# Kernel optimization log

Measured on AMD Instinct MI355X. Metric: run time of the kernel, lower is better.

Reference implementation:

```python
import jax, jax.numpy as jnp
import numpy as np
from jax import lax

B, N, D = 8, 1024, 2
MAX_ITERS = 100
REG = 0.1
INNER = 10  # convergence check cadence (cpt % 10 == 0 in the torch code)
TOL = 1e-3


def setup_inputs() -> dict:
    key = jax.random.key(0)
    k1, k2, k3, k4 = jax.random.split(key, 4)
    return {
        "coord1": jax.random.normal(k1, (B, N, D), jnp.float32),
        "prob1": jax.random.uniform(k2, (B, N), jnp.float32),
        "coord2": jax.random.normal(k3, (B, N, D), jnp.float32),
        "prob2": jax.random.uniform(k4, (B, N), jnp.float32),
    }


def _pairwise_sq(x, y):
    # squared euclidean distance, [B, N, N]; same math as the torch cat/broadcast version
    return jnp.sum((x[:, :, None, :] - y[:, None, :, :]) ** 2, axis=-1)


def _sinkhorn(a, b, M):
    bsz, n = a.shape
    a = a[..., None]                      # [B, n, 1]
    b = b[..., None]                      # [B, n, 1]
    K = jnp.exp(-M / REG)                 # [B, n, n]
    Kt = jnp.swapaxes(K, 1, 2)
    u0 = jnp.full((bsz, n, 1), 1.0 / n, M.dtype)
    v0 = jnp.full((bsz, n, 1), 1.0 / n, M.dtype)
    P0 = u0 * K * jnp.swapaxes(v0, 1, 2)
    done0 = jnp.array(False)

    def inner(c, _):
        u, v, done = c
        KtU = jnp.matmul(Kt, u)           # [B, n, 1]
        v1 = b / KtU
        u1 = a / jnp.matmul(K, v1)
        bad = jnp.any(KtU == 0) | ~(jnp.all(jnp.isfinite(u1)) & jnp.all(jnp.isfinite(v1)))
        ok = ~(done | bad)                # freeze updates after break (numerical error)
        return (jnp.where(ok, u1, u), jnp.where(ok, v1, v), done | bad), None

    def outer(c, _):
        u, v, P, done = c
        (u, v, done2), _ = lax.scan(inner, (u, v, done), None, length=INNER)
        Pn = u * K * jnp.swapaxes(v, 1, 2)
        upd = ~done2                      # skip P update if bad/converged already
        conv = jnp.max(jnp.abs(P - Pn)) < TOL
        P = jnp.where(upd, Pn, P)
        return (u, v, P, done2 | (upd & conv)), None

    (_, _, P, _), _ = lax.scan(outer, (u0, v0, P0, done0), None, length=MAX_ITERS // INNER)
    return P


def reference(coord1, prob1, coord2, prob2):
    M = _pairwise_sq(coord1, coord2)
    M = M / jnp.max(M, axis=(1, 2), keepdims=True)
    a = prob1 + 1e-8
    a = a / jnp.sum(a, axis=1, keepdims=True)
    bb = prob2 + 1e-8
    bb = bb / jnp.sum(bb, axis=1, keepdims=True)
    return _sinkhorn(a, bb, M)
```

## Files before the change

### kernel.cpp

```cpp
#include <hip/hip_runtime.h>
#include <hip/hip_fp16.h>

#define NPTS 1024
#define BATCH 8
#define BPB 32
#define NBLOCKS (BATCH * BPB)
#define NTHREADS 512
#define WPB 8
#define RPW 4
#define KCH 16
#define KP  8

#define SCOPE_AGENT __HIP_MEMORY_SCOPE_AGENT

typedef unsigned long long ull;

constexpr float REG_ = 0.1f;
constexpr float LOG2E = 1.4426950408889634f;
constexpr unsigned POISON = 0xAAAAAAAAu;

__device__ __forceinline__ float wave_sum(float x) {
    #pragma unroll
    for (int off = 32; off; off >>= 1) x += __shfl_xor(x, off);
    return x;
}
__device__ __forceinline__ float wave_max(float x) {
    #pragma unroll
    for (int off = 32; off; off >>= 1) x = fmaxf(x, __shfl_xor(x, off));
    return x;
}

__global__ __launch_bounds__(NTHREADS, 2) void sinkhorn_fused(
    const float2* __restrict__ c1g, const float* __restrict__ p1g,
    const float2* __restrict__ c2g, const float* __restrict__ p2g,
    float* __restrict__ out, unsigned* __restrict__ cnt_all,
    int* __restrict__ mmw_all, ull* __restrict__ upk_all,
    ull* __restrict__ vpk_all)
{
    const int tid  = threadIdx.x;
    const int lane = tid & 63;
    const int w    = tid >> 6;
    const int bid  = blockIdx.x & (BATCH - 1);
    const int sub  = blockIdx.x >> 3;
    const int gb   = bid << 10;
    const int r0   = sub * 32 + w * RPW;

    unsigned* cnt = cnt_all + bid * 32;
    int*      mmw = mmw_all + bid * 32;
    ull* upk = upk_all + (gb >> 1);
    ull* vpk = vpk_all + (gb >> 1);

    __shared__ float xe[NPTS];
    __shared__ float red[WPB];
    __shared__ float smax;

    float s1 = 0.f, s2 = 0.f;
    #pragma unroll
    for (int k = 0; k < KCH; ++k) {
        int t = lane + 64 * k;
        s1 += p1g[gb + t] + 1e-8f;
        s2 += p2g[gb + t] + 1e-8f;
    }
    s1 = wave_sum(s1);
    s2 = wave_sum(s2);

    float rc1x[RPW], rc1y[RPW], rc2x[RPW], rc2y[RPW], pa[RPW], pb[RPW];
    #pragma unroll
    for (int i = 0; i < RPW; ++i) {
        float2 c1 = c1g[gb + r0 + i];
        float2 c2 = c2g[gb + r0 + i];
        rc1x[i] = c1.x; rc1y[i] = c1.y;
        rc2x[i] = c2.x; rc2y[i] = c2.y;
        pa[i] = (p1g[gb + r0 + i] + 1e-8f) / s1;
        pb[i] = (p2g[gb + r0 + i] + 1e-8f) / s2;
    }

    float m = 0.f;
    #pragma unroll
    for (int k = 0; k < KCH; ++k) {
        float2 c = c2g[gb + lane + 64 * k];
        #pragma unroll
        for (int i = 0; i < RPW; ++i) {
            float dx = rc1x[i] - c.x, dy = rc1y[i] - c.y;
            m = fmaxf(m, dx * dx + dy * dy);
        }
    }
    m = wave_max(m);
    if (lane == 0) red[w] = m;
    __syncthreads();

    unsigned tgt = POISON + BPB;
    if (tid == 0) {
        float bm = red[0];
        #pragma unroll
        for (int i = 1; i < WPB; ++i) bm = fmaxf(bm, red[i]);
        __hip_atomic_fetch_max(mmw, (int)__float_as_uint(bm),
                               __ATOMIC_RELAXED, SCOPE_AGENT);
        asm volatile("s_waitcnt vmcnt(0)" ::: "memory");
        __hip_atomic_fetch_add(cnt, 1u, __ATOMIC_RELAXED, SCOPE_AGENT);
        while ((int)(__hip_atomic_load(cnt, __ATOMIC_RELAXED, SCOPE_AGENT) - tgt) < 0) {}
        smax = __uint_as_float((unsigned)
            __hip_atomic_load(mmw, __ATOMIC_RELAXED, SCOPE_AGENT));
    }
    __syncthreads();
    const float mmax = smax;
    const float nIL2 = -LOG2E / (REG_ * mmax);

    __half2 Kupk[RPW][KP], Kvpk[RPW][KP];
    #pragma unroll
    for (int p = 0; p < KP; ++p) {
        float2 cA = c2g[gb + lane + 128 * p];
        float2 cB = c2g[gb + lane + 128 * p + 64];
        #pragma unroll
        for (int i = 0; i < RPW; ++i) {
            float dxa = rc1x[i] - cA.x, dya = rc1y[i] - cA.y;
            float dxb = rc1x[i] - cB.x, dyb = rc1y[i] - cB.y;
            Kupk[i][p] = __floats2half2_rn(exp2f(nIL2 * (dxa * dxa + dya * dya)),
                                           exp2f(nIL2 * (dxb * dxb + dyb * dyb)));
        }
        float2 cC = c1g[gb + lane + 128 * p];
        float2 cD = c1g[gb + lane + 128 * p + 64];
        #pragma unroll
        for (int i = 0; i < RPW; ++i) {
            float dxa = rc2x[i] - cC.x, dya = rc2y[i] - cC.y;
            float dxb = rc2x[i] - cD.x, dyb = rc2y[i] - cD.y;
            Kvpk[i][p] = __floats2half2_rn(exp2f(nIL2 * (dxa * dxa + dya * dya)),
                                           exp2f(nIL2 * (dxb * dxb + dyb * dyb)));
        }
    }

    const int sa = (w << 6) + lane;
    float accu[RPW];
    float vcp[KCH];
    for (int it = 0; it < 10; ++it) {
        float acc[RPW] = {0.f, 0.f, 0.f, 0.f};
        if (it == 0) {
            #pragma unroll
            for (int p = 0; p < KP; ++p)
                #pragma unroll
                for (int i = 0; i < RPW; ++i) {
                    float2 kf = __half22float2(Kvpk[i][p]);
                    acc[i] += kf.x + kf.y;
                }
            #pragma unroll
            for (int i = 0; i < RPW; ++i) acc[i] *= (1.0f / NPTS);
        } else {
            #pragma unroll
            for (int p = 0; p < KP; ++p) {
                float x0 = xe[128 * p + lane];
                float x1 = xe[128 * p + 64 + lane];
                #pragma unroll
                for (int i = 0; i < RPW; ++i) {
                    float2 kf = __half22float2(Kvpk[i][p]);
                    acc[i] = fmaf(kf.x, x0, fmaf(kf.y, x1, acc[i]));
                }
            }
        }
        #pragma unroll
        for (int i = 0; i < RPW; ++i) acc[i] = wave_sum(acc[i]);
        if (lane == 0) {
            float v0 = pb[0] / acc[0], v1 = pb[1] / acc[1];
            float v2 = pb[2] / acc[2], v3 = pb[3] / acc[3];
            __hip_atomic_store(&vpk[r0 >> 1],
                ((ull)__float_as_uint(v1) << 32) | __float_as_uint(v0),
                __ATOMIC_RELAXED, SCOPE_AGENT);
            __hip_atomic_store(&vpk[(r0 >> 1) + 1],
                ((ull)__float_as_uint(v3) << 32) | __float_as_uint(v2),
                __ATOMIC_RELAXED, SCOPE_AGENT);
        }
        __syncthreads();
        tgt += BPB;
        if (tid == 0) {
            __hip_atomic_fetch_add(cnt, 1u, __ATOMIC_RELAXED, SCOPE_AGENT);
            while ((int)(__hip_atomic_load(cnt, __ATOMIC_RELAXED, SCOPE_AGENT) - tgt) < 0) {}
        }
        __syncthreads();
        {
            ull r = __hip_atomic_load(&vpk[sa], __ATOMIC_RELAXED, SCOPE_AGENT);
            ((float2*)xe)[sa] = make_float2(__uint_as_float((unsigned)r),
                                            __uint_as_float((unsigned)(r >> 32)));
        }
        __syncthreads();

        #pragma unroll
        for (int i = 0; i < RPW; ++i) accu[i] = 0.f;
        #pragma unroll
        for (int p = 0; p < KP; ++p) {
            float x0 = xe[128 * p + lane];
            float x1 = xe[128 * p + 64 + lane];
            if (it == 9) { vcp[2 * p] = x0; vcp[2 * p + 1] = x1; }
            #pragma unroll
            for (int i = 0; i < RPW; ++i) {
                float2 kf = __half22float2(Kupk[i][p]);
                accu[i] = fmaf(kf.x, x0, fmaf(kf.y, x1, accu[i]));
            }
        }
        #pragma unroll
        for (int i = 0; i < RPW; ++i) accu[i] = wave_sum(accu[i]);
        if (it < 9) {
            if (lane == 0) {
                float u0 = pa[0] / accu[0], u1 = pa[1] / accu[1];
                float u2 = pa[2] / accu[2], u3 = pa[3] / accu[3];
                __hip_atomic_store(&upk[r0 >> 1],
                    ((ull)__float_as_uint(u1) << 32) | __float_as_uint(u0),
                    __ATOMIC_RELAXED, SCOPE_AGENT);
                __hip_atomic_store(&upk[(r0 >> 1) + 1],
                    ((ull)__float_as_uint(u3) << 32) | __float_as_uint(u2),
                    __ATOMIC_RELAXED, SCOPE_AGENT);
            }
            __syncthreads();
            tgt += BPB;
            if (tid == 0) {
                __hip_atomic_fetch_add(cnt, 1u, __ATOMIC_RELAXED, SCOPE_AGENT);
                while ((int)(__hip_atomic_load(cnt, __ATOMIC_RELAXED, SCOPE_AGENT) - tgt) < 0) {}
            }
            __syncthreads();
            ull r = __hip_atomic_load(&upk[sa], __ATOMIC_RELAXED, SCOPE_AGENT);
            ((float2*)xe)[sa] = make_float2(__uint_as_float((unsigned)r),
                                            __uint_as_float((unsigned)(r >> 32)));
            __syncthreads();
        }
    }

    float rowu[RPW];
    #pragma unroll
    for (int i = 0; i < RPW; ++i) rowu[i] = pa[i] / accu[i];
    const long ob = ((long)bid << 20) + ((long)r0 << 10);
    #pragma unroll
    for (int p = 0; p < KP; ++p) {
        #pragma unroll
        for (int i = 0; i < RPW; ++i) {
            float2 kf = __half22float2(Kupk[i][p]);
            __builtin_nontemporal_store(rowu[i] * kf.x * vcp[2 * p],
                &out[ob + (i << 10) + 128 * p + lane]);
            __builtin_nontemporal_store(rowu[i] * kf.y * vcp[2 * p + 1],
                &out[ob + (i << 10) + 128 * p + 64 + lane]);
        }
    }
}

extern "C" void kernel_launch(void* const* d_in, const int* in_sizes, int n_in,
                              void* d_out, int out_size, void* d_ws, size_t ws_size,
                              hipStream_t stream) {
    const float2* c1 = (const float2*)d_in[0];
    const float*  p1 = (const float*)d_in[1];
    const float2* c2 = (const float2*)d_in[2];
    const float*  p2 = (const float*)d_in[3];
    float* out = (float*)d_out;

    unsigned* cnt = (unsigned*)d_ws;
    int*      mmw = (int*)((char*)d_ws + 1024);
    ull* upk = (ull*)((char*)d_ws + 2048);
    ull* vpk = upk + BATCH * NPTS / 2;

    sinkhorn_fused<<<NBLOCKS, NTHREADS, 0, stream>>>(c1, p1, c2, p2, out,
                                                     cnt, mmw, upk, vpk);
}
```

Before: 120.3 us.

## Replace counter barriers with tagged per-element flags and double-buffered shared vectors

Drops the per-batch atomic counter barrier and its three block syncs per half-iteration. Each u/v value is now published as a 64-bit word that carries an iteration tag, and every thread spins only on the two elements it needs. The shared exchange buffer is double-buffered, so a single __syncthreads is enough per exchange. This takes counter contention and serialized barrier latency off the critical path, at the cost of many more polling loads. It also assumes the workspace contents never accidentally match the tags (it depends on workspace initialisation state across calls).

```diff
diff --git a/kernel.cpp b/kernel.cpp
--- a/kernel.cpp
+++ b/kernel.cpp
@@ -17,7 +17,7 @@
 
 constexpr float REG_ = 0.1f;
 constexpr float LOG2E = 1.4426950408889634f;
-constexpr unsigned POISON = 0xAAAAAAAAu;
+constexpr unsigned MTAG = 0xBEEFu;
 
 __device__ __forceinline__ float wave_sum(float x) {
     #pragma unroll
@@ -28,14 +28,22 @@
     #pragma unroll
     for (int off = 32; off; off >>= 1) x = fmaxf(x, __shfl_xor(x, off));
     return x;
+}
+__device__ __forceinline__ ull pk(float v, unsigned tag) {
+    return ((ull)__float_as_uint(v) << 32) | (ull)tag;
+}
+__device__ __forceinline__ ull aload(const ull* p) {
+    return __hip_atomic_load(p, __ATOMIC_RELAXED, SCOPE_AGENT);
+}
+__device__ __forceinline__ void astore(ull* p, ull v) {
+    __hip_atomic_store(p, v, __ATOMIC_RELAXED, SCOPE_AGENT);
 }
 
 __global__ __launch_bounds__(NTHREADS, 2) void sinkhorn_fused(
     const float2* __restrict__ c1g, const float* __restrict__ p1g,
     const float2* __restrict__ c2g, const float* __restrict__ p2g,
-    float* __restrict__ out, unsigned* __restrict__ cnt_all,
-    int* __restrict__ mmw_all, ull* __restrict__ upk_all,
-    ull* __restrict__ vpk_all)
+    float* __restrict__ out, ull* __restrict__ mx_all,
+    ull* __restrict__ vat_all, ull* __restrict__ uat_all)
 {
     const int tid  = threadIdx.x;
     const int lane = tid & 63;
@@ -45,14 +53,12 @@
     const int gb   = bid << 10;
     const int r0   = sub * 32 + w * RPW;
 
-    unsigned* cnt = cnt_all + bid * 32;
-    int*      mmw = mmw_all + bid * 32;
-    ull* upk = upk_all + (gb >> 1);
-    ull* vpk = vpk_all + (gb >> 1);
-
-    __shared__ float xe[NPTS];
+    ull* mx  = mx_all  + bid * 32;
+    ull* vat = vat_all + gb;
+    ull* uat = uat_all + gb;
+
+    __shared__ float xe[2][NPTS];
     __shared__ float red[WPB];
-    __shared__ float smax;
 
     float s1 = 0.f, s2 = 0.f;
     #pragma unroll
@@ -88,22 +94,19 @@
     m = wave_max(m);
     if (lane == 0) red[w] = m;
     __syncthreads();
-
-    unsigned tgt = POISON + BPB;
     if (tid == 0) {
         float bm = red[0];
         #pragma unroll
         for (int i = 1; i < WPB; ++i) bm = fmaxf(bm, red[i]);
-        __hip_atomic_fetch_max(mmw, (int)__float_as_uint(bm),
-                               __ATOMIC_RELAXED, SCOPE_AGENT);
-        asm volatile("s_waitcnt vmcnt(0)" ::: "memory");
-        __hip_atomic_fetch_add(cnt, 1u, __ATOMIC_RELAXED, SCOPE_AGENT);
-        while ((int)(__hip_atomic_load(cnt, __ATOMIC_RELAXED, SCOPE_AGENT) - tgt) < 0) {}
-        smax = __uint_as_float((unsigned)
-            __hip_atomic_load(mmw, __ATOMIC_RELAXED, SCOPE_AGENT));
-    }
-    __syncthreads();
-    const float mmax = smax;
+        astore(mx + sub, pk(bm, MTAG));
+    }
+    float mmax;
+    {
+        const ull* p = mx + (lane & 31);
+        ull r = aload(p);
+        while ((unsigned)r != MTAG) r = aload(p);
+        mmax = wave_max(__uint_as_float((unsigned)(r >> 32)));
+    }
     const float nIL2 = -LOG2E / (REG_ * mmax);
 
     __half2 Kupk[RPW][KP], Kvpk[RPW][KP];
@@ -129,10 +132,13 @@
         }
     }
 
-    const int sa = (w << 6) + lane;
+    const int j2 = 2 * tid;
+    int cb = 0;
     float accu[RPW];
     float vcp[KCH];
     for (int it = 0; it < 10; ++it) {
+        const unsigned tg = (unsigned)(it + 1);
+
         float acc[RPW] = {0.f, 0.f, 0.f, 0.f};
         if (it == 0) {
             #pragma unroll
@@ -147,8 +153,8 @@
         } else {
             #pragma unroll
             for (int p = 0; p < KP; ++p) {
-                float x0 = xe[128 * p + lane];
-                float x1 = xe[128 * p + 64 + lane];
+                float x0 = xe[cb][128 * p + lane];
+                float x1 = xe[cb][128 * p + 64 + lane];
                 #pragma unroll
                 for (int i = 0; i < RPW; ++i) {
                     float2 kf = __half22float2(Kvpk[i][p]);
@@ -158,36 +164,27 @@
         }
         #pragma unroll
         for (int i = 0; i < RPW; ++i) acc[i] = wave_sum(acc[i]);
-        if (lane == 0) {
-            float v0 = pb[0] / acc[0], v1 = pb[1] / acc[1];
-            float v2 = pb[2] / acc[2], v3 = pb[3] / acc[3];
-            __hip_atomic_store(&vpk[r0 >> 1],
-                ((ull)__float_as_uint(v1) << 32) | __float_as_uint(v0),
-                __ATOMIC_RELAXED, SCOPE_AGENT);
-            __hip_atomic_store(&vpk[(r0 >> 1) + 1],
-                ((ull)__float_as_uint(v3) << 32) | __float_as_uint(v2),
-                __ATOMIC_RELAXED, SCOPE_AGENT);
+        if (lane < RPW) {
+            float num = lane == 0 ? pb[0] : lane == 1 ? pb[1] : lane == 2 ? pb[2] : pb[3];
+            float den = lane == 0 ? acc[0] : lane == 1 ? acc[1] : lane == 2 ? acc[2] : acc[3];
+            astore(vat + r0 + lane, pk(num / den, tg));
+        }
+        {
+            ull a = aload(vat + j2), b = aload(vat + j2 + 1);
+            while ((unsigned)a != tg) a = aload(vat + j2);
+            while ((unsigned)b != tg) b = aload(vat + j2 + 1);
+            xe[cb ^ 1][j2]     = __uint_as_float((unsigned)(a >> 32));
+            xe[cb ^ 1][j2 + 1] = __uint_as_float((unsigned)(b >> 32));
         }
         __syncthreads();
-        tgt += BPB;
-        if (tid == 0) {
-            __hip_atomic_fetch_add(cnt, 1u, __ATOMIC_RELAXED, SCOPE_AGENT);
-            while ((int)(__hip_atomic_load(cnt, __ATOMIC_RELAXED, SCOPE_AGENT) - tgt) < 0) {}
-        }
-        __syncthreads();
-        {
-            ull r = __hip_atomic_load(&vpk[sa], __ATOMIC_RELAXED, SCOPE_AGENT);
-            ((float2*)xe)[sa] = make_float2(__uint_as_float((unsigned)r),
-                                            __uint_as_float((unsigned)(r >> 32)));
-        }
-        __syncthreads();
+        cb ^= 1;
 
         #pragma unroll
         for (int i = 0; i < RPW; ++i) accu[i] = 0.f;
         #pragma unroll
         for (int p = 0; p < KP; ++p) {
-            float x0 = xe[128 * p + lane];
-            float x1 = xe[128 * p + 64 + lane];
+            float x0 = xe[cb][128 * p + lane];
+            float x1 = xe[cb][128 * p + 64 + lane];
             if (it == 9) { vcp[2 * p] = x0; vcp[2 * p + 1] = x1; }
             #pragma unroll
             for (int i = 0; i < RPW; ++i) {
@@ -198,27 +195,18 @@
         #pragma unroll
         for (int i = 0; i < RPW; ++i) accu[i] = wave_sum(accu[i]);
         if (it < 9) {
-            if (lane == 0) {
-                float u0 = pa[0] / accu[0], u1 = pa[1] / accu[1];
-                float u2 = pa[2] / accu[2], u3 = pa[3] / accu[3];
-                __hip_atomic_store(&upk[r0 >> 1],
-                    ((ull)__float_as_uint(u1) << 32) | __float_as_uint(u0),
-                    __ATOMIC_RELAXED, SCOPE_AGENT);
-                __hip_atomic_store(&upk[(r0 >> 1) + 1],
-                    ((ull)__float_as_uint(u3) << 32) | __float_as_uint(u2),
-                    __ATOMIC_RELAXED, SCOPE_AGENT);
+            if (lane < RPW) {
+                float num = lane == 0 ? pa[0] : lane == 1 ? pa[1] : lane == 2 ? pa[2] : pa[3];
+                float den = lane == 0 ? accu[0] : lane == 1 ? accu[1] : lane == 2 ? accu[2] : accu[3];
+                astore(uat + r0 + lane, pk(num / den, tg));
             }
+            ull a = aload(uat + j2), b = aload(uat + j2 + 1);
+            while ((unsigned)a != tg) a = aload(uat + j2);
+            while ((unsigned)b != tg) b = aload(uat + j2 + 1);
+            xe[cb ^ 1][j2]     = __uint_as_float((unsigned)(a >> 32));
+            xe[cb ^ 1][j2 + 1] = __uint_as_float((unsigned)(b >> 32));
             __syncthreads();
-            tgt += BPB;
-            if (tid == 0) {
-                __hip_atomic_fetch_add(cnt, 1u, __ATOMIC_RELAXED, SCOPE_AGENT);
-                while ((int)(__hip_atomic_load(cnt, __ATOMIC_RELAXED, SCOPE_AGENT) - tgt) < 0) {}
-            }
-            __syncthreads();
-            ull r = __hip_atomic_load(&upk[sa], __ATOMIC_RELAXED, SCOPE_AGENT);
-            ((float2*)xe)[sa] = make_float2(__uint_as_float((unsigned)r),
-                                            __uint_as_float((unsigned)(r >> 32)));
-            __syncthreads();
+            cb ^= 1;
         }
     }
 
@@ -248,11 +236,10 @@
     const float*  p2 = (const float*)d_in[3];
     float* out = (float*)d_out;
 
-    unsigned* cnt = (unsigned*)d_ws;
-    int*      mmw = (int*)((char*)d_ws + 1024);
-    ull* upk = (ull*)((char*)d_ws + 2048);
-    ull* vpk = upk + BATCH * NPTS / 2;
+    ull* mx  = (ull*)d_ws;
+    ull* vat = (ull*)((char*)d_ws + 2048);
+    ull* uat = vat + BATCH * NPTS;
 
     sinkhorn_fused<<<NBLOCKS, NTHREADS, 0, stream>>>(c1, p1, c2, p2, out,
-                                                     cnt, mmw, upk, vpk);
-}
+                                                     mx, vat, uat);
+}
```

Result: slower. 157.5 us (+30.9%).

## Split per-batch grid barrier counter into four padded counters polled by one wave

Applied to the files above, without the earlier changes.

Replaces the single per-batch atomic barrier counter with four counters, each on its own 128-byte slot and each shared by eight blocks. Waiting is done by lanes of wave 0 polling all four counters in parallel, so fewer atomic increments land on the same address. The per-row u/v divisions and packed stores are also split across two lanes instead of one. The aim is less atomic serialisation at the barrier, at the cost of more polling traffic and a new workspace layout.

```diff
diff --git a/kernel.cpp b/kernel.cpp
--- a/kernel.cpp
+++ b/kernel.cpp
@@ -10,6 +10,7 @@
 #define RPW 4
 #define KCH 16
 #define KP  8
+#define NCTR 4
 
 #define SCOPE_AGENT __HIP_MEMORY_SCOPE_AGENT
 
@@ -28,14 +29,23 @@
     #pragma unroll
     for (int off = 32; off; off >>= 1) x = fmaxf(x, __shfl_xor(x, off));
     return x;
+}
+__device__ __forceinline__ ull aload(const ull* p) {
+    return __hip_atomic_load(p, __ATOMIC_RELAXED, SCOPE_AGENT);
+}
+__device__ __forceinline__ void astore(ull* p, ull v) {
+    __hip_atomic_store(p, v, __ATOMIC_RELAXED, SCOPE_AGENT);
+}
+__device__ __forceinline__ unsigned aload32(const unsigned* p) {
+    return __hip_atomic_load(p, __ATOMIC_RELAXED, SCOPE_AGENT);
 }
 
 __global__ __launch_bounds__(NTHREADS, 2) void sinkhorn_fused(
     const float2* __restrict__ c1g, const float* __restrict__ p1g,
     const float2* __restrict__ c2g, const float* __restrict__ p2g,
     float* __restrict__ out, unsigned* __restrict__ cnt_all,
-    int* __restrict__ mmw_all, ull* __restrict__ upk_all,
-    ull* __restrict__ vpk_all)
+    int* __restrict__ mmw_all, unsigned* __restrict__ pc_all,
+    ull* __restrict__ upk_all, ull* __restrict__ vpk_all)
 {
     const int tid  = threadIdx.x;
     const int lane = tid & 63;
@@ -47,6 +57,7 @@
 
     unsigned* cnt = cnt_all + bid * 32;
     int*      mmw = mmw_all + bid * 32;
+    unsigned* pc  = pc_all  + bid * 128;
     ull* upk = upk_all + (gb >> 1);
     ull* vpk = vpk_all + (gb >> 1);
 
@@ -89,7 +100,6 @@
     if (lane == 0) red[w] = m;
     __syncthreads();
 
-    unsigned tgt = POISON + BPB;
     if (tid == 0) {
         float bm = red[0];
         #pragma unroll
@@ -98,7 +108,8 @@
                                __ATOMIC_RELAXED, SCOPE_AGENT);
         asm volatile("s_waitcnt vmcnt(0)" ::: "memory");
         __hip_atomic_fetch_add(cnt, 1u, __ATOMIC_RELAXED, SCOPE_AGENT);
-        while ((int)(__hip_atomic_load(cnt, __ATOMIC_RELAXED, SCOPE_AGENT) - tgt) < 0) {}
+        unsigned mtgt = POISON + BPB;
+        while ((int)(aload32(cnt) - mtgt) < 0) {}
         smax = __uint_as_float((unsigned)
             __hip_atomic_load(mmw, __ATOMIC_RELAXED, SCOPE_AGENT));
     }
@@ -128,6 +139,24 @@
                                            exp2f(nIL2 * (dxb * dxb + dyb * dyb)));
         }
     }
+
+    const int myctr = (sub >> 3) << 5;
+    unsigned ptgt = POISON;
+    auto arrive_wait = [&]() {
+        __syncthreads();
+        if (tid == 0)
+            __hip_atomic_fetch_add(pc + myctr, 1u, __ATOMIC_RELAXED, SCOPE_AGENT);
+        ptgt += 8;
+        if (w == 0) {
+            const unsigned* cp = pc + (lane << 5);
+            bool ok = lane >= NCTR;
+            if (!ok) ok = (int)(aload32(cp) - ptgt) >= 0;
+            while (!__all(ok)) {
+                if (lane < NCTR) ok = (int)(aload32(cp) - ptgt) >= 0;
+            }
+        }
+        __syncthreads();
+    };
 
     const int sa = (w << 6) + lane;
     float accu[RPW];
@@ -158,25 +187,15 @@
         }
         #pragma unroll
         for (int i = 0; i < RPW; ++i) acc[i] = wave_sum(acc[i]);
-        if (lane == 0) {
-            float v0 = pb[0] / acc[0], v1 = pb[1] / acc[1];
-            float v2 = pb[2] / acc[2], v3 = pb[3] / acc[3];
-            __hip_atomic_store(&vpk[r0 >> 1],
-                ((ull)__float_as_uint(v1) << 32) | __float_as_uint(v0),
-                __ATOMIC_RELAXED, SCOPE_AGENT);
-            __hip_atomic_store(&vpk[(r0 >> 1) + 1],
-                ((ull)__float_as_uint(v3) << 32) | __float_as_uint(v2),
-                __ATOMIC_RELAXED, SCOPE_AGENT);
-        }
-        __syncthreads();
-        tgt += BPB;
-        if (tid == 0) {
-            __hip_atomic_fetch_add(cnt, 1u, __ATOMIC_RELAXED, SCOPE_AGENT);
-            while ((int)(__hip_atomic_load(cnt, __ATOMIC_RELAXED, SCOPE_AGENT) - tgt) < 0) {}
-        }
-        __syncthreads();
+        if (lane < 2) {
+            float n0 = lane ? pb[2] : pb[0], n1 = lane ? pb[3] : pb[1];
+            float d0 = lane ? acc[2] : acc[0], d1 = lane ? acc[3] : acc[1];
+            astore(&vpk[(r0 >> 1) + lane],
+                   ((ull)__float_as_uint(n1 / d1) << 32) | __float_as_uint(n0 / d0));
+        }
+        arrive_wait();
         {
-            ull r = __hip_atomic_load(&vpk[sa], __ATOMIC_RELAXED, SCOPE_AGENT);
+            ull r = aload(&vpk[sa]);
             ((float2*)xe)[sa] = make_float2(__uint_as_float((unsigned)r),
                                             __uint_as_float((unsigned)(r >> 32)));
         }
@@ -198,24 +217,14 @@
         #pragma unroll
         for (int i = 0; i < RPW; ++i) accu[i] = wave_sum(accu[i]);
         if (it < 9) {
-            if (lane == 0) {
-                float u0 = pa[0] / accu[0], u1 = pa[1] / accu[1];
-                float u2 = pa[2] / accu[2], u3 = pa[3] / accu[3];
-                __hip_atomic_store(&upk[r0 >> 1],
-                    ((ull)__float_as_uint(u1) << 32) | __float_as_uint(u0),
-                    __ATOMIC_RELAXED, SCOPE_AGENT);
-                __hip_atomic_store(&upk[(r0 >> 1) + 1],
-                    ((ull)__float_as_uint(u3) << 32) | __float_as_uint(u2),
-                    __ATOMIC_RELAXED, SCOPE_AGENT);
-            }
-            __syncthreads();
-            tgt += BPB;
-            if (tid == 0) {
-                __hip_atomic_fetch_add(cnt, 1u, __ATOMIC_RELAXED, SCOPE_AGENT);
-                while ((int)(__hip_atomic_load(cnt, __ATOMIC_RELAXED, SCOPE_AGENT) - tgt) < 0) {}
-            }
-            __syncthreads();
-            ull r = __hip_atomic_load(&upk[sa], __ATOMIC_RELAXED, SCOPE_AGENT);
+            if (lane < 2) {
+                float n0 = lane ? pa[2] : pa[0], n1 = lane ? pa[3] : pa[1];
+                float d0 = lane ? accu[2] : accu[0], d1 = lane ? accu[3] : accu[1];
+                astore(&upk[(r0 >> 1) + lane],
+                       ((ull)__float_as_uint(n1 / d1) << 32) | __float_as_uint(n0 / d0));
+            }
+            arrive_wait();
+            ull r = aload(&upk[sa]);
             ((float2*)xe)[sa] = make_float2(__uint_as_float((unsigned)r),
                                             __uint_as_float((unsigned)(r >> 32)));
             __syncthreads();
@@ -250,9 +259,10 @@
 
     unsigned* cnt = (unsigned*)d_ws;
     int*      mmw = (int*)((char*)d_ws + 1024);
-    ull* upk = (ull*)((char*)d_ws + 2048);
+    unsigned* pc  = (unsigned*)((char*)d_ws + 2048);
+    ull* upk = (ull*)((char*)d_ws + 6144);
     ull* vpk = upk + BATCH * NPTS / 2;
 
     sinkhorn_fused<<<NBLOCKS, NTHREADS, 0, stream>>>(c1, p1, c2, p2, out,
-                                                     cnt, mmw, upk, vpk);
-}
+                                                     cnt, mmw, pc, upk, vpk);
+}
```

Result: slower. 138.5 us (+15.1%).
